# Performance work log

Hardware: AMD Instinct MI355X
Metric: run time of the kernel (lower is better)

## Reference

```python
import jax, jax.numpy as jnp
import numpy as np

NEG_INF = jnp.float32(-1e30)  # stand-in for -inf; relu(-inf) == relu(-1e30) == 0


def setup_inputs() -> dict:
    key = jax.random.key(0)
    ks = jax.random.split(key, 8)
    B, S, E = 4, 4096, 512
    query = jax.random.normal(ks[0], (B, S, E), dtype=jnp.float32)
    k_in = jax.random.normal(ks[1], (B, S, E), dtype=jnp.float32)
    v_in = jax.random.normal(ks[2], (B, S, E), dtype=jnp.float32)
    mask = jax.random.randint(ks[3], (B, S, S), 0, 2) > 0  # bool [B,S,S]
    scale = 1.0 / np.sqrt(E)
    W1 = jax.random.uniform(ks[4], (E, E), jnp.float32, -scale, scale)
    b1 = jax.random.uniform(ks[5], (E,), jnp.float32, -scale, scale)
    W2 = jax.random.uniform(ks[6], (E, E), jnp.float32, -scale, scale)
    b2 = jax.random.uniform(ks[7], (E,), jnp.float32, -scale, scale)
    return {"query": query, "key": k_in, "value": v_in, "mask": mask,
            "W1": W1, "b1": b1, "W2": W2, "b2": b2}


def reference(query, key, value, mask, W1, b1, W2, b2):
    # key projection: nn.Linear -> x @ W.T + b
    k = jnp.einsum('bse,fe->bsf', key, W1) + b1
    # raw dot-product correlation scores [B, S, S]
    scores = jnp.einsum('bqe,bke->bqk', query, k)
    # module forces mask[:, :, 0] = True, then fills ~mask with -inf
    m = mask.at[:, :, 0].set(True)
    scores = jnp.where(m, scores, NEG_INF)
    # ReLU instead of softmax (no normalization); dropout is identity in eval
    alpha = jax.nn.relu(scores)
    # value projection then AV matmul
    v = jnp.einsum('bse,fe->bsf', value, W2) + b2
    out = jnp.einsum('bqk,bke->bqe', alpha, v)
    return out
```

## Files before the change

### kernel.cpp

```cpp
#include <hip/hip_runtime.h>
#include <cstdint>


typedef __bf16 bf16x8 __attribute__((ext_vector_type(8)));
typedef float f32x4 __attribute__((ext_vector_type(4)));

__device__ __forceinline__ unsigned short f2bf(float f) {
  unsigned int u = __float_as_uint(f);
  u += 0x7fffu + ((u >> 16) & 1u);
  return (unsigned short)(u >> 16);
}

__device__ __forceinline__ void async_load16(const void* g, void* l) {
  __builtin_amdgcn_global_load_lds(
      (const __attribute__((address_space(1))) unsigned int*)(uintptr_t)g,
      (__attribute__((address_space(3))) unsigned int*)(unsigned int)(uintptr_t)l,
      16, 0, 0);
}

__global__ void cvt_f32_bf16(const float* __restrict__ in,
                             unsigned short* __restrict__ out, int n4) {
  int i = blockIdx.x * blockDim.x + threadIdx.x;
  if (i < n4) {
    float4 f = ((const float4*)in)[i];
    ushort4 o;
    o.x = f2bf(f.x); o.y = f2bf(f.y); o.z = f2bf(f.z); o.w = f2bf(f.w);
    ((ushort4*)out)[i] = o;
  }
}

__global__ void pack_mask(const int* __restrict__ m, unsigned int* __restrict__ bits) {
  const int lane = threadIdx.x & 63;
  const size_t wid = ((size_t)blockIdx.x * blockDim.x + threadIdx.x) >> 6;
  const size_t base = wid * 256;
  unsigned long long bl[4];
#pragma unroll
  for (int c = 0; c < 4; ++c) {
    size_t e = base + (size_t)c * 64 + lane;
    int col = (int)(e & 4095);
    bl[c] = __ballot((m[e] != 0) || (col == 0));
  }
  if (lane < 8)
    bits[base / 32 + lane] = (unsigned int)(bl[lane >> 1] >> ((lane & 1) * 32));
}

template <int EPI>
__global__ void __launch_bounds__(256)
gemm_bt(const unsigned short* __restrict__ A, const unsigned short* __restrict__ B,
        void* __restrict__ Cout, const float* __restrict__ bias,
        const unsigned int* __restrict__ mbits,
        int M, int N, int K,
        long long strA, long long strB, long long strC, long long strM) {
  __shared__ unsigned short sA[128 * 32];
  __shared__ unsigned short sB[128 * 32];

  const int tid  = threadIdx.x;
  const int lane = tid & 63;
  const int wave = tid >> 6;
  const int bz   = blockIdx.z;
  const int tn0  = blockIdx.x * 128;
  const int tm0  = blockIdx.y * 128;

  const unsigned short* Ab = A + (size_t)bz * strA;
  const unsigned short* Bb = B + (size_t)bz * strB;

  const int ldrow = lane >> 2;
  const int lcol  = (lane & 3) * 8;
  const int wm = (wave >> 1) * 64;
  const int wn = (wave & 1) * 64;
  const int lr = lane & 15;
  const int lq = lane >> 4;

  f32x4 acc[4][4] = {};

  for (int k0 = 0; k0 < K; k0 += 32) {
#pragma unroll
    for (int l = 0; l < 2; ++l) {
      const int row = wave * 32 + l * 16;
      async_load16(Ab + (size_t)(tm0 + row + ldrow) * K + (k0 + lcol), &sA[row * 32]);
      async_load16(Bb + (size_t)(tn0 + row + ldrow) * K + (k0 + lcol), &sB[row * 32]);
    }
    __syncthreads();

    bf16x8 af[4], bfr[4];
#pragma unroll
    for (int t = 0; t < 4; ++t) {
      af[t]  = *(const bf16x8*)&sA[(wm + t * 16 + lr) * 32 + lq * 8];
      bfr[t] = *(const bf16x8*)&sB[(wn + t * 16 + lr) * 32 + lq * 8];
    }
#pragma unroll
    for (int mt = 0; mt < 4; ++mt)
#pragma unroll
      for (int nt = 0; nt < 4; ++nt)
        acc[mt][nt] = __builtin_amdgcn_mfma_f32_16x16x32_bf16(af[mt], bfr[nt],
                                                              acc[mt][nt], 0, 0, 0);
    __syncthreads();
  }

#pragma unroll
  for (int mt = 0; mt < 4; ++mt) {
#pragma unroll
    for (int r = 0; r < 4; ++r) {
      const int m = tm0 + wm + mt * 16 + lq * 4 + r;
      unsigned long long w64 = 0;
      if constexpr (EPI == 2) {
        w64 = *(const unsigned long long*)&mbits[(size_t)bz * strM +
                                                 (size_t)m * (N >> 5) + ((tn0 + wn) >> 5)];
      }
#pragma unroll
      for (int nt = 0; nt < 4; ++nt) {
        const int n = tn0 + wn + nt * 16 + lr;
        float v = acc[mt][nt][r];
        if constexpr (EPI == 0) {
          v += bias[n];
          ((unsigned short*)Cout)[(size_t)bz * strC + (size_t)m * N + n] = f2bf(v);
        } else if constexpr (EPI == 1) {
          v += bias[m];
          ((unsigned short*)Cout)[(size_t)bz * strC + (size_t)m * N + n] = f2bf(v);
        } else if constexpr (EPI == 2) {
          v = ((w64 >> (nt * 16 + lr)) & 1ull) ? fmaxf(v, 0.f) : 0.f;
          ((unsigned short*)Cout)[(size_t)bz * strC + (size_t)m * N + n] = f2bf(v);
        } else {
          ((float*)Cout)[(size_t)bz * strC + (size_t)m * N + n] = v;
        }
      }
    }
  }
}

extern "C" void kernel_launch(void* const* d_in, const int* in_sizes, int n_in,
                              void* d_out, int out_size, void* d_ws, size_t ws_size,
                              hipStream_t stream) {
  const float* query = (const float*)d_in[0];
  const float* key   = (const float*)d_in[1];
  const float* value = (const float*)d_in[2];
  const int*   mask  = (const int*)d_in[3];
  const float* W1    = (const float*)d_in[4];
  const float* b1    = (const float*)d_in[5];
  const float* W2    = (const float*)d_in[6];
  const float* b2    = (const float*)d_in[7];
  float* out = (float*)d_out;

  constexpr int B = 4, S = 4096, E = 512;
  constexpr long long BSE = (long long)B * S * E;
  constexpr long long SE  = (long long)S * E;
  constexpr long long SS  = (long long)S * S;
  constexpr long long BSS = (long long)B * S * S;
  constexpr long long EE  = (long long)E * E;

  char* ws = (char*)d_ws;
  unsigned short* Qb   = (unsigned short*)ws;  ws += BSE * 2;
  unsigned short* Kb   = (unsigned short*)ws;  ws += BSE * 2;
  unsigned short* Vb   = (unsigned short*)ws;  ws += BSE * 2;
  unsigned short* W1b  = (unsigned short*)ws;  ws += EE * 2;
  unsigned short* W2b  = (unsigned short*)ws;  ws += EE * 2;
  unsigned short* Kp   = (unsigned short*)ws;  ws += BSE * 2;
  unsigned short* Vpt  = (unsigned short*)ws;  ws += BSE * 2;
  unsigned short* alph = (unsigned short*)ws;  ws += BSS * 2;
  unsigned int*   mbit = (unsigned int*)ws;    ws += BSS / 8;

  cvt_f32_bf16<<<dim3(BSE / 1024), 256, 0, stream>>>(query, Qb, (int)(BSE / 4));
  cvt_f32_bf16<<<dim3(BSE / 1024), 256, 0, stream>>>(key,   Kb, (int)(BSE / 4));
  cvt_f32_bf16<<<dim3(BSE / 1024), 256, 0, stream>>>(value, Vb, (int)(BSE / 4));
  cvt_f32_bf16<<<dim3(EE / 1024),  256, 0, stream>>>(W1, W1b, (int)(EE / 4));
  cvt_f32_bf16<<<dim3(EE / 1024),  256, 0, stream>>>(W2, W2b, (int)(EE / 4));

  pack_mask<<<dim3((int)(BSS / 1024)), 256, 0, stream>>>(mask, mbit);

  gemm_bt<0><<<dim3(E / 128, (B * S) / 128, 1), 256, 0, stream>>>(
      Kb, W1b, Kp, b1, nullptr, B * S, E, E, 0, 0, 0, 0);

  gemm_bt<1><<<dim3(S / 128, E / 128, B), 256, 0, stream>>>(
      W2b, Vb, Vpt, b2, nullptr, E, S, E, 0, SE, SE, 0);

  gemm_bt<2><<<dim3(S / 128, S / 128, B), 256, 0, stream>>>(
      Qb, Kp, alph, nullptr, mbit, S, S, E, SE, SE, SS, SS / 32);

  gemm_bt<3><<<dim3(E / 128, S / 128, B), 256, 0, stream>>>(
      alph, Vpt, out, nullptr, nullptr, S, E, S, SS, SE, SE, 0);
}
```

Before: 729.2 us.

## Split-K the AV GEMM across two halves and merge conversion launches

```diff
diff --git a/kernel.cpp b/kernel.cpp
--- a/kernel.cpp
+++ b/kernel.cpp
@@ -18,15 +18,31 @@
       16, 0, 0);
 }
 
-__global__ void cvt_f32_bf16(const float* __restrict__ in,
-                             unsigned short* __restrict__ out, int n4) {
+__global__ void cvt3_f32_bf16(const float* __restrict__ i0, const float* __restrict__ i1,
+                              const float* __restrict__ i2,
+                              unsigned short* __restrict__ o0, unsigned short* __restrict__ o1,
+                              unsigned short* __restrict__ o2, int n4) {
   int i = blockIdx.x * blockDim.x + threadIdx.x;
-  if (i < n4) {
-    float4 f = ((const float4*)in)[i];
-    ushort4 o;
-    o.x = f2bf(f.x); o.y = f2bf(f.y); o.z = f2bf(f.z); o.w = f2bf(f.w);
-    ((ushort4*)out)[i] = o;
-  }
+  if (i >= n4) return;
+  const float* in = (blockIdx.y == 0) ? i0 : (blockIdx.y == 1) ? i1 : i2;
+  unsigned short* out = (blockIdx.y == 0) ? o0 : (blockIdx.y == 1) ? o1 : o2;
+  float4 f = ((const float4*)in)[i];
+  ushort4 o;
+  o.x = f2bf(f.x); o.y = f2bf(f.y); o.z = f2bf(f.z); o.w = f2bf(f.w);
+  ((ushort4*)out)[i] = o;
+}
+
+__global__ void cvt2_f32_bf16(const float* __restrict__ i0, const float* __restrict__ i1,
+                              unsigned short* __restrict__ o0, unsigned short* __restrict__ o1,
+                              int n4) {
+  int i = blockIdx.x * blockDim.x + threadIdx.x;
+  if (i >= n4) return;
+  const float* in = (blockIdx.y == 0) ? i0 : i1;
+  unsigned short* out = (blockIdx.y == 0) ? o0 : o1;
+  float4 f = ((const float4*)in)[i];
+  ushort4 o;
+  o.x = f2bf(f.x); o.y = f2bf(f.y); o.z = f2bf(f.z); o.w = f2bf(f.w);
+  ((ushort4*)out)[i] = o;
 }
 
 __global__ void pack_mask(const int* __restrict__ m, unsigned int* __restrict__ bits) {
@@ -42,6 +58,17 @@
   }
   if (lane < 8)
     bits[base / 32 + lane] = (unsigned int)(bl[lane >> 1] >> ((lane & 1) * 32));
+}
+
+__global__ void reduce_split(const float* __restrict__ p, float* __restrict__ out,
+                             long long half_elems, int n4) {
+  int i = blockIdx.x * blockDim.x + threadIdx.x;
+  if (i >= n4) return;
+  float4 a = ((const float4*)p)[i];
+  float4 b = ((const float4*)(p + half_elems))[i];
+  float4 r;
+  r.x = a.x + b.x; r.y = a.y + b.y; r.z = a.z + b.z; r.w = a.w + b.w;
+  ((float4*)out)[i] = r;
 }
 
 template <int EPI>
@@ -61,8 +88,15 @@
   const int tn0  = blockIdx.x * 128;
   const int tm0  = blockIdx.y * 128;
 
-  const unsigned short* Ab = A + (size_t)bz * strA;
-  const unsigned short* Bb = B + (size_t)bz * strB;
+  int bb = bz, kbeg = 0, kend = K;
+  if constexpr (EPI == 3) {
+    bb = bz & 3;
+    kbeg = (bz >> 2) * (K >> 1);
+    kend = kbeg + (K >> 1);
+  }
+
+  const unsigned short* Ab = A + (size_t)bb * strA;
+  const unsigned short* Bb = B + (size_t)bb * strB;
 
   const int ldrow = lane >> 2;
   const int lcol  = (lane & 3) * 8;
@@ -73,7 +107,7 @@
 
   f32x4 acc[4][4] = {};
 
-  for (int k0 = 0; k0 < K; k0 += 32) {
+  for (int k0 = kbeg; k0 < kend; k0 += 32) {
 #pragma unroll
     for (int l = 0; l < 2; ++l) {
       const int row = wave * 32 + l * 16;
@@ -158,12 +192,12 @@
   unsigned short* Vpt  = (unsigned short*)ws;  ws += BSE * 2;
   unsigned short* alph = (unsigned short*)ws;  ws += BSS * 2;
   unsigned int*   mbit = (unsigned int*)ws;    ws += BSS / 8;
-
-  cvt_f32_bf16<<<dim3(BSE / 1024), 256, 0, stream>>>(query, Qb, (int)(BSE / 4));
-  cvt_f32_bf16<<<dim3(BSE / 1024), 256, 0, stream>>>(key,   Kb, (int)(BSE / 4));
-  cvt_f32_bf16<<<dim3(BSE / 1024), 256, 0, stream>>>(value, Vb, (int)(BSE / 4));
-  cvt_f32_bf16<<<dim3(EE / 1024),  256, 0, stream>>>(W1, W1b, (int)(EE / 4));
-  cvt_f32_bf16<<<dim3(EE / 1024),  256, 0, stream>>>(W2, W2b, (int)(EE / 4));
+  float*          part = (float*)ws;           ws += BSE * 4 * 2;
+
+  cvt3_f32_bf16<<<dim3(BSE / 1024, 3), 256, 0, stream>>>(
+      query, key, value, Qb, Kb, Vb, (int)(BSE / 4));
+  cvt2_f32_bf16<<<dim3(EE / 1024, 2), 256, 0, stream>>>(
+      W1, W2, W1b, W2b, (int)(EE / 4));
 
   pack_mask<<<dim3((int)(BSS / 1024)), 256, 0, stream>>>(mask, mbit);
 
@@ -176,6 +210,9 @@
   gemm_bt<2><<<dim3(S / 128, S / 128, B), 256, 0, stream>>>(
       Qb, Kp, alph, nullptr, mbit, S, S, E, SE, SE, SS, SS / 32);
 
-  gemm_bt<3><<<dim3(E / 128, S / 128, B), 256, 0, stream>>>(
-      alph, Vpt, out, nullptr, nullptr, S, E, S, SS, SE, SE, 0);
-}
+  gemm_bt<3><<<dim3(E / 128, S / 128, 2 * B), 256, 0, stream>>>(
+      alph, Vpt, part, nullptr, nullptr, S, E, S, SS, SE, SE, 0);
+
+  reduce_split<<<dim3((int)(BSE / 1024)), 256, 0, stream>>>(
+      part, out, BSE, (int)(BSE / 4));
+}
```

After: 744.8 us. 1.02x slower.
